# Kernel tuning notes

Measured on AMD Instinct MI355X. Metric: run time of the kernel, lower is better.

Reference implementation:

```python
import jax, jax.numpy as jnp
import numpy as np

NUM_SCALES = 4
ENC = 64
KMAX = 16
DT = 0.005  # base_time_constant; original code's (undefined) self.dt interpreted as this


def setup_inputs() -> dict:
    key = jax.random.key(0)
    ks = jax.random.split(key, 5)
    events = jax.random.normal(ks[0], (2, 2, 32, 32, 64), dtype=jnp.float32)
    # matches torch.logspace(-3, -1, num_scales)
    time_constants = jnp.logspace(-3.0, -1.0, NUM_SCALES).astype(jnp.float32)
    temporal_kernels = jax.random.normal(ks[1], (NUM_SCALES, ENC, KMAX), dtype=jnp.float32)
    w1 = jax.random.normal(ks[2], (2 * NUM_SCALES, NUM_SCALES), dtype=jnp.float32) * 0.1
    b1 = jnp.zeros((2 * NUM_SCALES,), dtype=jnp.float32)
    w2 = jax.random.normal(ks[3], (NUM_SCALES, 2 * NUM_SCALES), dtype=jnp.float32) * 0.1
    b2 = jnp.zeros((NUM_SCALES,), dtype=jnp.float32)
    return {"events": events, "time_constants": time_constants,
            "temporal_kernels": temporal_kernels, "w1": w1, "b1": b1, "w2": w2, "b2": b2}


def reference(events, time_constants, temporal_kernels, w1, b1, w2, b2):
    B, C, H, W, T = events.shape
    k = min(KMAX, T)
    # decay kernels per scale: [S, k], normalized to sum 1
    t_idx = jnp.arange(k, dtype=jnp.float32)
    decay = jnp.exp(-t_idx[None, :] * DT / time_constants[:, None])
    decay = decay / decay.sum(axis=-1, keepdims=True)
    # combined learnable kernels: [S, E, k]
    combined = decay[:, None, :] * temporal_kernels[:, :, :k]

    Cf = C * H * W
    # one batched cross-correlation (torch F.conv1d semantics == lax conv, no flip)
    x = events.reshape(B * Cf, 1, T)                       # [B*Cf, 1, T]
    kern = combined.reshape(NUM_SCALES * ENC, 1, k)        # [S*E, 1, k]
    out = jax.lax.conv_general_dilated(
        x, kern, window_strides=(1,), padding=[(k // 2, k // 2)],
        dimension_numbers=("NCH", "OIH", "NCH"))           # [B*Cf, S*E, T+1]
    Tp = out.shape[-1]
    # [B, E, S, Cf, Tp] matching torch stack order (enc at dim1, scale at dim2)
    feats = out.reshape(B, Cf, NUM_SCALES, ENC, Tp).transpose(0, 3, 2, 1, 4)

    # torch .var() is unbiased -> ddof=1
    feature_variance = feats.var(axis=-1, ddof=1).mean(axis=(1, 3))  # [B, S]
    h = jax.nn.relu(feature_variance @ w1.T + b1)
    attn = jax.nn.softmax(h @ w2.T + b2, axis=-1)                    # [B, S]

    encoded = (feats * attn[:, None, :, None, None]).sum(axis=2)     # [B, E, Cf, Tp]
    return encoded
```

## Files before the change

### kernel.cpp

```cpp
#include <hip/hip_runtime.h>

#define KK 16
#define SS 4
#define EE 64
#define BB 2
#define DT_CONST 0.005f

typedef float f32x4 __attribute__((ext_vector_type(4)));
typedef short bf16x8 __attribute__((ext_vector_type(8)));

#define WS_WK_F 34816

__global__ void __launch_bounds__(512, 1) kA_gram(const float* __restrict__ events,
                                                  float* __restrict__ ws) {
    __shared__ float xs[16][97];
    __shared__ float S1L[16][16];
    __shared__ float part[16][136];
    const int tid = threadIdx.x;

    if (tid < 256) {
        const float4* src = reinterpret_cast<const float4*>(
            events + (size_t)blockIdx.x * 1024);
        float4 v = src[tid];
        int r = tid >> 4, c0 = ((tid & 15) << 2) + 8;
        xs[r][c0] = v.x; xs[r][c0+1] = v.y; xs[r][c0+2] = v.z; xs[r][c0+3] = v.w;
    }
    for (int idx = tid; idx < 16 * 33; idx += 512) {
        int rr = idx / 33, k = idx % 33;
        xs[rr][(k < 8) ? k : (k + 64)] = 0.f;
    }
    __syncthreads();

    const int r   = tid >> 5;
    const int c   = tid & 31;
    const int lag = c >> 1;
    const int h   = c & 1;
    const int off = h * 33;
    const float inv65 = 1.f / 65.f;

    {
        float s = 0.f;
#pragma unroll
        for (int j = 0; j < 32; ++j) s += xs[r][lag + off + j];
        if (!h) s += xs[r][lag + 32];
        s += __shfl_xor(s, 1, 64);
        if (!h) S1L[r][lag] = s;
    }
    __syncthreads();

    {
        float C = 0.f;
#pragma unroll
        for (int j = 0; j < 32; ++j) C += xs[r][off + j] * xs[r][off + j + lag];
        if (!h) C += xs[r][32] * xs[r][32 + lag];
        {
            float Ct = C + __shfl_xor(C, 1, 64);
            if (!h) part[r][lag] = Ct - S1L[r][0] * S1L[r][lag] * inv65;
        }
#pragma unroll
        for (int d1 = 1; d1 <= 15; ++d1) {
            const int add = d1 + off + 32 - h;
            const int rem = d1 - 1 + off;
            C += xs[r][add] * xs[r][add + lag] - xs[r][rem] * xs[r][rem + lag];
            if (lag + d1 <= 15) {
                float Ct = C + __shfl_xor(C, 1, 64);
                if (!h) {
                    int p = 16 * d1 - ((d1 * (d1 - 1)) >> 1) + lag;
                    part[r][p] = Ct - S1L[r][d1] * S1L[r][d1 + lag] * inv65;
                }
            } else {
            }
        }
    }
    __syncthreads();

    if (tid < 136) {
        float g = 0.f;
#pragma unroll
        for (int rr = 0; rr < 16; ++rr) g += part[rr][tid];
        ws[((size_t)((blockIdx.x >> 7) * 136 + tid)) * 128 + (blockIdx.x & 127)] = g;
    }
}

__global__ void __launch_bounds__(256, 1) kM_mlp(const float* __restrict__ tc,
        const float* __restrict__ tk, const float* __restrict__ w1,
        const float* __restrict__ b1, const float* __restrict__ w2,
        const float* __restrict__ b2, float* __restrict__ ws) {
    __shared__ float Gf[2 * 256];
    __shared__ float combL[SS * EE * KK];
    __shared__ float fvL[BB * SS];
    __shared__ float attnL[BB][SS];
    const int tid = threadIdx.x;

    for (int v = tid; v < 272; v += 256) {
        int b = (v >= 136) ? 1 : 0;
        int p = v - b * 136;
        int pp = p, d1 = 0;
        while (pp >= KK - d1) { pp -= KK - d1; ++d1; }
        int d2 = d1 + pp;
        const float4* rp = reinterpret_cast<const float4*>(ws + (size_t)v * 128);
        float acc = 0.f;
#pragma unroll
        for (int i = 0; i < 32; ++i) { float4 q = rp[i]; acc += (q.x + q.y) + (q.z + q.w); }
        Gf[b * 256 + d1 * KK + d2] = acc;
        Gf[b * 256 + d2 * KK + d1] = acc;
    }
    {
        int s = tid >> 6;
        float inv = DT_CONST / tc[s];
        float dk[KK]; float dsum = 0.f;
#pragma unroll
        for (int j = 0; j < KK; ++j) { dk[j] = expf(-(float)j * inv); dsum += dk[j]; }
        float rn = 1.f / dsum;
#pragma unroll
        for (int i = 0; i < 4; ++i) {
            float4 v = reinterpret_cast<const float4*>(tk + tid * KK)[i];
            combL[tid * KK + 4*i + 0] = dk[4*i + 0] * rn * v.x;
            combL[tid * KK + 4*i + 1] = dk[4*i + 1] * rn * v.y;
            combL[tid * KK + 4*i + 2] = dk[4*i + 2] * rn * v.z;
            combL[tid * KK + 4*i + 3] = dk[4*i + 3] * rn * v.w;
        }
    }
    __syncthreads();
    {
        float cvec[KK];
#pragma unroll
        for (int i = 0; i < 4; ++i) {
            float4 v = reinterpret_cast<const float4*>(combL + tid * KK)[i];
            cvec[4*i] = v.x; cvec[4*i+1] = v.y; cvec[4*i+2] = v.z; cvec[4*i+3] = v.w;
        }
        float acc0 = 0.f, acc1 = 0.f;
#pragma unroll
        for (int d1 = 0; d1 < KK; ++d1) {
            float cd1 = cvec[d1];
            float t0 = 0.5f * Gf[d1 * KK + d1] * cd1;
            float t1 = 0.5f * Gf[256 + d1 * KK + d1] * cd1;
#pragma unroll
            for (int d2 = d1 + 1; d2 < KK; ++d2) {
                t0 += Gf[d1 * KK + d2] * cvec[d2];
                t1 += Gf[256 + d1 * KK + d2] * cvec[d2];
            }
            acc0 += 2.f * cd1 * t0;
            acc1 += 2.f * cd1 * t1;
        }
#pragma unroll
        for (int sft = 1; sft < 64; sft <<= 1) {
            acc0 += __shfl_xor(acc0, sft, 64);
            acc1 += __shfl_xor(acc1, sft, 64);
        }
        if ((tid & 63) == 0) {
            const float scale = 1.f / 8388608.f;
            fvL[(tid >> 6)]     = acc0 * scale;
            fvL[4 + (tid >> 6)] = acc1 * scale;
        }
    }
    __syncthreads();
    if (tid < 2) {
        int b = tid;
        float h[8];
#pragma unroll
        for (int i = 0; i < 8; ++i) {
            float a = b1[i];
#pragma unroll
            for (int s = 0; s < SS; ++s) a += fvL[b * SS + s] * w1[i * SS + s];
            h[i] = a > 0.f ? a : 0.f;
        }
        float lg[SS]; float mx = -1e30f;
#pragma unroll
        for (int s = 0; s < SS; ++s) {
            float a = b2[s];
#pragma unroll
            for (int i = 0; i < 8; ++i) a += h[i] * w2[s * 8 + i];
            lg[s] = a; mx = fmaxf(mx, a);
        }
        float se = 0.f;
#pragma unroll
        for (int s = 0; s < SS; ++s) { lg[s] = expf(lg[s] - mx); se += lg[s]; }
#pragma unroll
        for (int s = 0; s < SS; ++s) attnL[b][s] = lg[s] / se;
    }
    __syncthreads();
    {
        unsigned short* wkp = reinterpret_cast<unsigned short*>(ws + WS_WK_F);
#pragma unroll
        for (int j = 0; j < 8; ++j) {
            int o = tid * 8 + j;
            int b = o >> 10, e = (o >> 4) & 63, k = o & 15;
            float a = 0.f;
#pragma unroll
            for (int s = 0; s < SS; ++s)
                a += attnL[b][s] * combL[(s * EE + e) * KK + k];
            unsigned int bits = __float_as_uint(a);
            unsigned short hh = (unsigned short)(bits >> 16);
            float hf = __uint_as_float(((unsigned int)hh) << 16);
            unsigned short ll = (unsigned short)(__float_as_uint(a - hf) >> 16);
            int base = b * 2048 + e * 32 + k;
            wkp[base]          = hh;   wkp[base + 16]        = 0;
            wkp[4096 + base]   = ll;   wkp[4096 + base + 16] = 0;
        }
    }
}

__global__ void __launch_bounds__(256, 8) kC_conv(const float* __restrict__ events,
                                                  const float* __restrict__ ws,
                                                  float* __restrict__ out) {
    __shared__ float xs[2][97];
    __shared__ __align__(16) unsigned short Bh[80 * 24 + 16];
    __shared__ __align__(16) unsigned short Bl[80 * 24 + 16];
    const int tid = threadIdx.x;
    const int bid = blockIdx.x;
    const int b   = bid >> 10;
    const int cf0 = (bid & 1023) << 1;
    const int w   = tid >> 6, l = tid & 63, llo = l & 15, lhi = l >> 4;

    for (int idx = tid; idx < 80 * 24 + 16; idx += 256) { Bh[idx] = 0; Bl[idx] = 0; }

    const unsigned short* wkp = reinterpret_cast<const unsigned short*>(ws + WS_WK_F);
    bf16x8 Ah = *reinterpret_cast<const bf16x8*>(wkp + b * 2048 + (w * 16 + llo) * 32 + 8 * lhi);
    bf16x8 Al = *reinterpret_cast<const bf16x8*>(wkp + 4096 + b * 2048 + (w * 16 + llo) * 32 + 8 * lhi);

    if (tid < 32) {
        float4 v = reinterpret_cast<const float4*>(
            events + ((size_t)b * 2048 + cf0) * 64)[tid];
        int rr = tid >> 4, c0 = ((tid & 15) << 2) + 8;
        xs[rr][c0] = v.x; xs[rr][c0+1] = v.y; xs[rr][c0+2] = v.z; xs[rr][c0+3] = v.w;
    }
    for (int idx = tid; idx < 66; idx += 256) {
        int rr = idx / 33, k = idx % 33;
        xs[rr][(k < 8) ? k : (k + 64)] = 0.f;
    }
    __syncthreads();

#pragma unroll 1
    for (int rr = 0; rr < 2; ++rr) {
#pragma unroll
        for (int q = 0; q < 5; ++q) {
            int idx = tid + q * 256;
            int t = idx >> 4, k = idx & 15;
            float x = xs[rr][t + k];
            unsigned int bits = __float_as_uint(x);
            unsigned short hh = (unsigned short)(bits >> 16);
            float hf = __uint_as_float(((unsigned int)hh) << 16);
            unsigned short ll = (unsigned short)(__float_as_uint(x - hf) >> 16);
            Bh[t * 24 + k] = hh;
            Bl[t * 24 + k] = ll;
        }
        __syncthreads();

        const size_t obase = ((size_t)(b * 64 + w * 16 + lhi * 4) * 2048 + (cf0 + rr)) * 65;
#pragma unroll
        for (int nt = 0; nt < 5; ++nt) {
            bf16x8 Xh = *reinterpret_cast<const bf16x8*>(Bh + (nt * 16 + llo) * 24 + 8 * lhi);
            bf16x8 Xl = *reinterpret_cast<const bf16x8*>(Bl + (nt * 16 + llo) * 24 + 8 * lhi);
            f32x4 acc = {0.f, 0.f, 0.f, 0.f};
            acc = __builtin_amdgcn_mfma_f32_16x16x32_bf16(Al, Xh, acc, 0, 0, 0);
            acc = __builtin_amdgcn_mfma_f32_16x16x32_bf16(Ah, Xl, acc, 0, 0, 0);
            acc = __builtin_amdgcn_mfma_f32_16x16x32_bf16(Ah, Xh, acc, 0, 0, 0);
            const int t0 = nt * 16 + llo;
            if (t0 < 65) {
#pragma unroll
                for (int i = 0; i < 4; ++i)
                    out[obase + (size_t)i * (2048 * 65) + t0] = acc[i];
            }
        }
        __syncthreads();
    }
}

extern "C" void kernel_launch(void* const* d_in, const int* in_sizes, int n_in,
                              void* d_out, int out_size, void* d_ws, size_t ws_size,
                              hipStream_t stream) {
    const float* events = (const float*)d_in[0];
    const float* tc     = (const float*)d_in[1];
    const float* tk     = (const float*)d_in[2];
    const float* w1     = (const float*)d_in[3];
    const float* b1     = (const float*)d_in[4];
    const float* w2     = (const float*)d_in[5];
    const float* b2     = (const float*)d_in[6];
    float* out = (float*)d_out;
    float* ws  = (float*)d_ws;

    hipLaunchKernelGGL(kA_gram, dim3(256),  dim3(512), 0, stream, events, ws);
    hipLaunchKernelGGL(kM_mlp,  dim3(1),    dim3(256), 0, stream, tc, tk, w1, b1, w2, b2, ws);
    hipLaunchKernelGGL(kC_conv, dim3(2048), dim3(256), 0, stream, events, ws, out);
}
```

Measured before the change: 37.95 us.

## Replace MFMA split-bf16 conv with fp32 register sliding-window conv and coalesced stores

The final convolution kernel drops the bf16 hi/lo split MFMA path and computes each output row in fp32 with a 16-tap sliding window held in registers. Each thread covers 16 time steps of one row. Results are staged in shared memory, then written to the output as contiguous float4 stores across a whole 64-row block, instead of scattered scalar stores. The mixing kernel now stores fp32 attention-weighted kernels instead of bf16 pairs. The change trades tensor-core math for plain FMA work, in exchange for fully coalesced writes to the large output.

Measured after the change: 41.47 us. 1.09x slower.

```diff
diff --git a/kernel.cpp b/kernel.cpp
--- a/kernel.cpp
+++ b/kernel.cpp
@@ -1,13 +1,13 @@
 #include <hip/hip_runtime.h>
 
+#define CF 2048
+#define TT 64
+#define TP 65
 #define KK 16
 #define SS 4
 #define EE 64
 #define BB 2
 #define DT_CONST 0.005f
-
-typedef float f32x4 __attribute__((ext_vector_type(4)));
-typedef short bf16x8 __attribute__((ext_vector_type(8)));
 
 #define WS_WK_F 34816
 
@@ -68,7 +68,6 @@
                     int p = 16 * d1 - ((d1 * (d1 - 1)) >> 1) + lag;
                     part[r][p] = Ct - S1L[r][d1] * S1L[r][d1 + lag] * inv65;
                 }
-            } else {
             }
         }
     }
@@ -181,7 +180,6 @@
     }
     __syncthreads();
     {
-        unsigned short* wkp = reinterpret_cast<unsigned short*>(ws + WS_WK_F);
 #pragma unroll
         for (int j = 0; j < 8; ++j) {
             int o = tid * 8 + j;
@@ -190,81 +188,82 @@
 #pragma unroll
             for (int s = 0; s < SS; ++s)
                 a += attnL[b][s] * combL[(s * EE + e) * KK + k];
-            unsigned int bits = __float_as_uint(a);
-            unsigned short hh = (unsigned short)(bits >> 16);
-            float hf = __uint_as_float(((unsigned int)hh) << 16);
-            unsigned short ll = (unsigned short)(__float_as_uint(a - hf) >> 16);
-            int base = b * 2048 + e * 32 + k;
-            wkp[base]          = hh;   wkp[base + 16]        = 0;
-            wkp[4096 + base]   = ll;   wkp[4096 + base + 16] = 0;
-        }
-    }
-}
-
-__global__ void __launch_bounds__(256, 8) kC_conv(const float* __restrict__ events,
+            ws[WS_WK_F + o] = a;
+        }
+    }
+}
+
+__global__ void __launch_bounds__(256, 4) kC_conv(const float* __restrict__ events,
                                                   const float* __restrict__ ws,
                                                   float* __restrict__ out) {
-    __shared__ float xs[2][97];
-    __shared__ __align__(16) unsigned short Bh[80 * 24 + 16];
-    __shared__ __align__(16) unsigned short Bl[80 * 24 + 16];
+    __shared__ float buf[64 * TP];
     const int tid = threadIdx.x;
-    const int bid = blockIdx.x;
-    const int b   = bid >> 10;
-    const int cf0 = (bid & 1023) << 1;
-    const int w   = tid >> 6, l = tid & 63, llo = l & 15, lhi = l >> 4;
-
-    for (int idx = tid; idx < 80 * 24 + 16; idx += 256) { Bh[idx] = 0; Bl[idx] = 0; }
-
-    const unsigned short* wkp = reinterpret_cast<const unsigned short*>(ws + WS_WK_F);
-    bf16x8 Ah = *reinterpret_cast<const bf16x8*>(wkp + b * 2048 + (w * 16 + llo) * 32 + 8 * lhi);
-    bf16x8 Al = *reinterpret_cast<const bf16x8*>(wkp + 4096 + b * 2048 + (w * 16 + llo) * 32 + 8 * lhi);
-
-    if (tid < 32) {
-        float4 v = reinterpret_cast<const float4*>(
-            events + ((size_t)b * 2048 + cf0) * 64)[tid];
-        int rr = tid >> 4, c0 = ((tid & 15) << 2) + 8;
-        xs[rr][c0] = v.x; xs[rr][c0+1] = v.y; xs[rr][c0+2] = v.z; xs[rr][c0+3] = v.w;
-    }
-    for (int idx = tid; idx < 66; idx += 256) {
-        int rr = idx / 33, k = idx % 33;
-        xs[rr][(k < 8) ? k : (k + 64)] = 0.f;
-    }
-    __syncthreads();
-
-#pragma unroll 1
-    for (int rr = 0; rr < 2; ++rr) {
-#pragma unroll
-        for (int q = 0; q < 5; ++q) {
-            int idx = tid + q * 256;
-            int t = idx >> 4, k = idx & 15;
-            float x = xs[rr][t + k];
-            unsigned int bits = __float_as_uint(x);
-            unsigned short hh = (unsigned short)(bits >> 16);
-            float hf = __uint_as_float(((unsigned int)hh) << 16);
-            unsigned short ll = (unsigned short)(__float_as_uint(x - hf) >> 16);
-            Bh[t * 24 + k] = hh;
-            Bl[t * 24 + k] = ll;
-        }
-        __syncthreads();
-
-        const size_t obase = ((size_t)(b * 64 + w * 16 + lhi * 4) * 2048 + (cf0 + rr)) * 65;
-#pragma unroll
-        for (int nt = 0; nt < 5; ++nt) {
-            bf16x8 Xh = *reinterpret_cast<const bf16x8*>(Bh + (nt * 16 + llo) * 24 + 8 * lhi);
-            bf16x8 Xl = *reinterpret_cast<const bf16x8*>(Bl + (nt * 16 + llo) * 24 + 8 * lhi);
-            f32x4 acc = {0.f, 0.f, 0.f, 0.f};
-            acc = __builtin_amdgcn_mfma_f32_16x16x32_bf16(Al, Xh, acc, 0, 0, 0);
-            acc = __builtin_amdgcn_mfma_f32_16x16x32_bf16(Ah, Xl, acc, 0, 0, 0);
-            acc = __builtin_amdgcn_mfma_f32_16x16x32_bf16(Ah, Xh, acc, 0, 0, 0);
-            const int t0 = nt * 16 + llo;
-            if (t0 < 65) {
-#pragma unroll
-                for (int i = 0; i < 4; ++i)
-                    out[obase + (size_t)i * (2048 * 65) + t0] = acc[i];
-            }
-        }
-        __syncthreads();
-    }
+    const int seg = tid >> 6;
+    const int r   = tid & 63;
+    const int c   = blockIdx.x;
+    const int be  = c >> 5;
+    const int rowg = (c << 6) + r;
+    const int b   = be >> 6;
+    const float* xr = events + (((size_t)b << 11) + (rowg & (CF - 1))) * TT;
+
+    float wk[KK];
+#pragma unroll
+    for (int i = 0; i < 4; ++i) {
+        float4 v = reinterpret_cast<const float4*>(ws + WS_WK_F + be * KK)[i];
+        wk[4*i] = v.x; wk[4*i+1] = v.y; wk[4*i+2] = v.z; wk[4*i+3] = v.w;
+    }
+
+    float win[32];
+    if (seg == 0) {
+#pragma unroll
+        for (int k = 0; k < 8; ++k) win[k] = 0.f;
+#pragma unroll
+        for (int k = 0; k < 6; ++k) {
+            float4 v = reinterpret_cast<const float4*>(xr)[k];
+            win[8+4*k] = v.x; win[9+4*k] = v.y; win[10+4*k] = v.z; win[11+4*k] = v.w;
+        }
+    } else if (seg == 3) {
+#pragma unroll
+        for (int k = 0; k < 6; ++k) {
+            float4 v = reinterpret_cast<const float4*>(xr + 40)[k];
+            win[4*k] = v.x; win[4*k+1] = v.y; win[4*k+2] = v.z; win[4*k+3] = v.w;
+        }
+#pragma unroll
+        for (int k = 24; k < 32; ++k) win[k] = 0.f;
+    } else {
+        const float* bp2 = xr + (seg == 1 ? 8 : 24);
+#pragma unroll
+        for (int k = 0; k < 8; ++k) {
+            float4 v = reinterpret_cast<const float4*>(bp2)[k];
+            win[4*k] = v.x; win[4*k+1] = v.y; win[4*k+2] = v.z; win[4*k+3] = v.w;
+        }
+    }
+
+    float acc[16];
+#pragma unroll
+    for (int i = 0; i < 16; ++i) acc[i] = 0.f;
+#pragma unroll
+    for (int dt = 0; dt < 16; ++dt) {
+        float w = wk[dt];
+#pragma unroll
+        for (int i = 0; i < 16; ++i) acc[i] += w * win[i + dt];
+    }
+    float acc16 = 0.f;
+    if (seg == 3) {
+#pragma unroll
+        for (int dt = 0; dt < 8; ++dt) acc16 += wk[dt] * win[16 + dt];
+    }
+
+    float* bp = buf + r * TP + seg * 16;
+#pragma unroll
+    for (int i = 0; i < 16; ++i) bp[i] = acc[i];
+    if (seg == 3) bp[16] = acc16;
+    __syncthreads();
+
+    const float4* bs = reinterpret_cast<const float4*>(buf);
+    float4* od = reinterpret_cast<float4*>(out + (size_t)c * (64 * TP));
+    for (int j = tid; j < 64 * TP / 4; j += 256)
+        od[j] = bs[j];
 }
 
 extern "C" void kernel_launch(void* const* d_in, const int* in_sizes, int n_in,
@@ -282,5 +281,5 @@
 
     hipLaunchKernelGGL(kA_gram, dim3(256),  dim3(512), 0, stream, events, ws);
     hipLaunchKernelGGL(kM_mlp,  dim3(1),    dim3(256), 0, stream, tc, tk, w1, b1, w2, b2, ws);
-    hipLaunchKernelGGL(kC_conv, dim3(2048), dim3(256), 0, stream, events, ws, out);
-}
+    hipLaunchKernelGGL(kC_conv, dim3(4096), dim3(256), 0, stream, events, ws, out);
+}
```

## Split gram kernel into more smaller blocks with four-way lag-sum lanes

Applied to the files above, without the earlier changes.

The gram/variance kernel now runs 1024 blocks of 256 threads, each handling 4 rows instead of 16. Each lag is summed by four lanes over 16-element segments with a two-step shuffle reduction, where before two lanes covered 32-element segments. The aim is better occupancy and shorter serial loops on the many-CU GPU. In exchange, the partial-sum buffer grows fourfold, so the single-block MLP kernel must read and reduce 512 partials per entry instead of 128.

After: 54.06 us. 1.42x slower.

```diff
diff --git a/kernel.cpp b/kernel.cpp
--- a/kernel.cpp
+++ b/kernel.cpp
@@ -9,76 +9,77 @@
 typedef float f32x4 __attribute__((ext_vector_type(4)));
 typedef short bf16x8 __attribute__((ext_vector_type(8)));
 
-#define WS_WK_F 34816
-
-__global__ void __launch_bounds__(512, 1) kA_gram(const float* __restrict__ events,
+#define WS_WK_F 139264
+
+__global__ void __launch_bounds__(256, 4) kA_gram(const float* __restrict__ events,
                                                   float* __restrict__ ws) {
-    __shared__ float xs[16][97];
-    __shared__ float S1L[16][16];
-    __shared__ float part[16][136];
+    __shared__ float xs[4][97];
+    __shared__ float S1L[4][16];
+    __shared__ float part[4][136];
     const int tid = threadIdx.x;
 
-    if (tid < 256) {
+    if (tid < 64) {
         const float4* src = reinterpret_cast<const float4*>(
-            events + (size_t)blockIdx.x * 1024);
+            events + (size_t)blockIdx.x * 256);
         float4 v = src[tid];
         int r = tid >> 4, c0 = ((tid & 15) << 2) + 8;
         xs[r][c0] = v.x; xs[r][c0+1] = v.y; xs[r][c0+2] = v.z; xs[r][c0+3] = v.w;
     }
-    for (int idx = tid; idx < 16 * 33; idx += 512) {
-        int rr = idx / 33, k = idx % 33;
+    if (tid < 132) {
+        int rr = tid / 33, k = tid % 33;
         xs[rr][(k < 8) ? k : (k + 64)] = 0.f;
     }
     __syncthreads();
 
-    const int r   = tid >> 5;
-    const int c   = tid & 31;
-    const int lag = c >> 1;
-    const int h   = c & 1;
-    const int off = h * 33;
+    const int r   = tid >> 6;
+    const int l   = tid & 63;
+    const int lag = l >> 2;
+    const int q   = l & 3;
+    const int off = q << 4;
     const float inv65 = 1.f / 65.f;
 
     {
         float s = 0.f;
 #pragma unroll
-        for (int j = 0; j < 32; ++j) s += xs[r][lag + off + j];
-        if (!h) s += xs[r][lag + 32];
+        for (int j = 0; j < 16; ++j) s += xs[r][lag + off + j];
+        if (q == 3) s += xs[r][lag + 64];
         s += __shfl_xor(s, 1, 64);
-        if (!h) S1L[r][lag] = s;
+        s += __shfl_xor(s, 2, 64);
+        if (q == 0) S1L[r][lag] = s;
     }
     __syncthreads();
 
     {
         float C = 0.f;
 #pragma unroll
-        for (int j = 0; j < 32; ++j) C += xs[r][off + j] * xs[r][off + j + lag];
-        if (!h) C += xs[r][32] * xs[r][32 + lag];
+        for (int j = 0; j < 16; ++j) C += xs[r][off + j] * xs[r][off + j + lag];
+        if (q == 3) C += xs[r][64] * xs[r][64 + lag];
         {
             float Ct = C + __shfl_xor(C, 1, 64);
-            if (!h) part[r][lag] = Ct - S1L[r][0] * S1L[r][lag] * inv65;
-        }
+            Ct += __shfl_xor(Ct, 2, 64);
+            if (q == 0) part[r][lag] = Ct - S1L[r][0] * S1L[r][lag] * inv65;
+        }
+        const int len = 16 + (q == 3 ? 1 : 0);
 #pragma unroll
         for (int d1 = 1; d1 <= 15; ++d1) {
-            const int add = d1 + off + 32 - h;
+            const int add = d1 - 1 + off + len;
             const int rem = d1 - 1 + off;
             C += xs[r][add] * xs[r][add + lag] - xs[r][rem] * xs[r][rem + lag];
             if (lag + d1 <= 15) {
                 float Ct = C + __shfl_xor(C, 1, 64);
-                if (!h) {
+                Ct += __shfl_xor(Ct, 2, 64);
+                if (q == 0) {
                     int p = 16 * d1 - ((d1 * (d1 - 1)) >> 1) + lag;
                     part[r][p] = Ct - S1L[r][d1] * S1L[r][d1 + lag] * inv65;
                 }
-            } else {
             }
         }
     }
     __syncthreads();
 
     if (tid < 136) {
-        float g = 0.f;
-#pragma unroll
-        for (int rr = 0; rr < 16; ++rr) g += part[rr][tid];
-        ws[((size_t)((blockIdx.x >> 7) * 136 + tid)) * 128 + (blockIdx.x & 127)] = g;
+        float g = part[0][tid] + part[1][tid] + part[2][tid] + part[3][tid];
+        ws[((size_t)((blockIdx.x >> 9) * 136 + tid)) * 512 + (blockIdx.x & 511)] = g;
     }
 }
 
@@ -98,10 +99,10 @@
         int pp = p, d1 = 0;
         while (pp >= KK - d1) { pp -= KK - d1; ++d1; }
         int d2 = d1 + pp;
-        const float4* rp = reinterpret_cast<const float4*>(ws + (size_t)v * 128);
+        const float4* rp = reinterpret_cast<const float4*>(ws + (size_t)v * 512);
         float acc = 0.f;
-#pragma unroll
-        for (int i = 0; i < 32; ++i) { float4 q = rp[i]; acc += (q.x + q.y) + (q.z + q.w); }
+#pragma unroll 16
+        for (int i = 0; i < 128; ++i) { float4 qv = rp[i]; acc += (qv.x + qv.y) + (qv.z + qv.w); }
         Gf[b * 256 + d1 * KK + d2] = acc;
         Gf[b * 256 + d2 * KK + d1] = acc;
     }
@@ -280,7 +281,7 @@
     float* out = (float*)d_out;
     float* ws  = (float*)d_ws;
 
-    hipLaunchKernelGGL(kA_gram, dim3(256),  dim3(512), 0, stream, events, ws);
+    hipLaunchKernelGGL(kA_gram, dim3(1024), dim3(256), 0, stream, events, ws);
     hipLaunchKernelGGL(kM_mlp,  dim3(1),    dim3(256), 0, stream, tc, tk, w1, b1, w2, b2, ws);
     hipLaunchKernelGGL(kC_conv, dim3(2048), dim3(256), 0, stream, events, ws, out);
 }
```

## Fuse MLP attention into conv kernel with LDS-staged coalesced output stores

Applied to the files above, without the earlier changes.

Merges the single-block MLP/attention kernel into the convolution kernel, so each of 512 blocks recomputes the Gram-based variance, softmax attention and the bf16 hi/lo weights in LDS instead of reading them from workspace, which removes one kernel launch and its serialization. Each block now handles 8 rows instead of 2. Conv results are staged in LDS and written out row-wise along time for coalescing, with the next row's bf16 split double-buffered. In exchange every block repeats the small MLP work and uses more LDS, which lowers occupancy.

Measured after the change: 37.25 us. Within noise of the previous version (-1.8%).

```diff
diff --git a/kernel.cpp b/kernel.cpp
--- a/kernel.cpp
+++ b/kernel.cpp
@@ -9,7 +9,6 @@
 typedef float f32x4 __attribute__((ext_vector_type(4)));
 typedef short bf16x8 __attribute__((ext_vector_type(8)));
 
-#define WS_WK_F 34816
 
 __global__ void __launch_bounds__(512, 1) kA_gram(const float* __restrict__ events,
                                                   float* __restrict__ ws) {
@@ -68,7 +67,6 @@
                     int p = 16 * d1 - ((d1 * (d1 - 1)) >> 1) + lag;
                     part[r][p] = Ct - S1L[r][d1] * S1L[r][d1 + lag] * inv65;
                 }
-            } else {
             }
         }
     }
@@ -82,19 +80,40 @@
     }
 }
 
-__global__ void __launch_bounds__(256, 1) kM_mlp(const float* __restrict__ tc,
+__global__ void __launch_bounds__(256, 2) kB5_main(
+        const float* __restrict__ events, const float* __restrict__ tc,
         const float* __restrict__ tk, const float* __restrict__ w1,
         const float* __restrict__ b1, const float* __restrict__ w2,
-        const float* __restrict__ b2, float* __restrict__ ws) {
-    __shared__ float Gf[2 * 256];
-    __shared__ float combL[SS * EE * KK];
-    __shared__ float fvL[BB * SS];
-    __shared__ float attnL[BB][SS];
+        const float* __restrict__ b2, const float* __restrict__ ws,
+        float* __restrict__ out) {
+    __shared__ float stage[2][4352];
+    __shared__ float xs[8 * 97];
+    __shared__ __align__(16) unsigned short wkh[64 * 32];
+    __shared__ __align__(16) unsigned short wkl[64 * 32];
+    __shared__ __align__(16) unsigned short Bh[2][1936];
+    __shared__ __align__(16) unsigned short Bl[2][1936];
+    float* Gf    = stage[0];
+    float* fvL   = stage[0] + 512;
+    float* combL = stage[1];
     const int tid = threadIdx.x;
-
+    const int bid = blockIdx.x;
+    const int b   = bid >> 8;
+    const int w   = tid >> 6, l = tid & 63, llo = l & 15, lhi = l >> 4;
+
+    for (int idx = tid; idx < 2 * 1936; idx += 256) { Bh[0][idx] = 0; Bl[0][idx] = 0; }
+    for (int idx = tid; idx < 8 * 33; idx += 256) {
+        int rr = idx / 33, k = idx % 33;
+        xs[rr * 97 + ((k < 8) ? k : (k + 64))] = 0.f;
+    }
+    if (tid < 128) {
+        float4 v = reinterpret_cast<const float4*>(events + (size_t)bid * 512)[tid];
+        int rr = tid >> 4, c0 = ((tid & 15) << 2) + 8;
+        xs[rr * 97 + c0] = v.x; xs[rr * 97 + c0 + 1] = v.y;
+        xs[rr * 97 + c0 + 2] = v.z; xs[rr * 97 + c0 + 3] = v.w;
+    }
     for (int v = tid; v < 272; v += 256) {
-        int b = (v >= 136) ? 1 : 0;
-        int p = v - b * 136;
+        int b2i = (v >= 136) ? 1 : 0;
+        int p  = v - b2i * 136;
         int pp = p, d1 = 0;
         while (pp >= KK - d1) { pp -= KK - d1; ++d1; }
         int d2 = d1 + pp;
@@ -102,8 +121,8 @@
         float acc = 0.f;
 #pragma unroll
         for (int i = 0; i < 32; ++i) { float4 q = rp[i]; acc += (q.x + q.y) + (q.z + q.w); }
-        Gf[b * 256 + d1 * KK + d2] = acc;
-        Gf[b * 256 + d2 * KK + d1] = acc;
+        Gf[(b2i * KK + d1) * KK + d2] = acc;
+        Gf[(b2i * KK + d2) * KK + d1] = acc;
     }
     {
         int s = tid >> 6;
@@ -122,6 +141,7 @@
         }
     }
     __syncthreads();
+
     {
         float cvec[KK];
 #pragma unroll
@@ -155,14 +175,17 @@
         }
     }
     __syncthreads();
-    if (tid < 2) {
-        int b = tid;
+
+    {
+        float fv[SS];
+#pragma unroll
+        for (int s = 0; s < SS; ++s) fv[s] = fvL[b * SS + s];
         float h[8];
 #pragma unroll
         for (int i = 0; i < 8; ++i) {
             float a = b1[i];
 #pragma unroll
-            for (int s = 0; s < SS; ++s) a += fvL[b * SS + s] * w1[i * SS + s];
+            for (int s = 0; s < SS; ++s) a += fv[s] * w1[i * SS + s];
             h[i] = a > 0.f ? a : 0.f;
         }
         float lg[SS]; float mx = -1e30f;
@@ -176,94 +199,98 @@
         float se = 0.f;
 #pragma unroll
         for (int s = 0; s < SS; ++s) { lg[s] = expf(lg[s] - mx); se += lg[s]; }
-#pragma unroll
-        for (int s = 0; s < SS; ++s) attnL[b][s] = lg[s] / se;
-    }
-    __syncthreads();
-    {
-        unsigned short* wkp = reinterpret_cast<unsigned short*>(ws + WS_WK_F);
-#pragma unroll
-        for (int j = 0; j < 8; ++j) {
-            int o = tid * 8 + j;
-            int b = o >> 10, e = (o >> 4) & 63, k = o & 15;
+        float attn[SS];
+#pragma unroll
+        for (int s = 0; s < SS; ++s) attn[s] = lg[s] / se;
+#pragma unroll
+        for (int j = 0; j < 4; ++j) {
+            int idx = tid * 4 + j;
+            int e = idx >> 4, k2 = idx & 15;
             float a = 0.f;
 #pragma unroll
             for (int s = 0; s < SS; ++s)
-                a += attnL[b][s] * combL[(s * EE + e) * KK + k];
+                a += attn[s] * combL[(s * EE + e) * KK + k2];
             unsigned int bits = __float_as_uint(a);
             unsigned short hh = (unsigned short)(bits >> 16);
             float hf = __uint_as_float(((unsigned int)hh) << 16);
             unsigned short ll = (unsigned short)(__float_as_uint(a - hf) >> 16);
-            int base = b * 2048 + e * 32 + k;
-            wkp[base]          = hh;   wkp[base + 16]        = 0;
-            wkp[4096 + base]   = ll;   wkp[4096 + base + 16] = 0;
-        }
-    }
-}
-
-__global__ void __launch_bounds__(256, 8) kC_conv(const float* __restrict__ events,
-                                                  const float* __restrict__ ws,
-                                                  float* __restrict__ out) {
-    __shared__ float xs[2][97];
-    __shared__ __align__(16) unsigned short Bh[80 * 24 + 16];
-    __shared__ __align__(16) unsigned short Bl[80 * 24 + 16];
-    const int tid = threadIdx.x;
-    const int bid = blockIdx.x;
-    const int b   = bid >> 10;
-    const int cf0 = (bid & 1023) << 1;
-    const int w   = tid >> 6, l = tid & 63, llo = l & 15, lhi = l >> 4;
-
-    for (int idx = tid; idx < 80 * 24 + 16; idx += 256) { Bh[idx] = 0; Bl[idx] = 0; }
-
-    const unsigned short* wkp = reinterpret_cast<const unsigned short*>(ws + WS_WK_F);
-    bf16x8 Ah = *reinterpret_cast<const bf16x8*>(wkp + b * 2048 + (w * 16 + llo) * 32 + 8 * lhi);
-    bf16x8 Al = *reinterpret_cast<const bf16x8*>(wkp + 4096 + b * 2048 + (w * 16 + llo) * 32 + 8 * lhi);
-
-    if (tid < 32) {
-        float4 v = reinterpret_cast<const float4*>(
-            events + ((size_t)b * 2048 + cf0) * 64)[tid];
-        int rr = tid >> 4, c0 = ((tid & 15) << 2) + 8;
-        xs[rr][c0] = v.x; xs[rr][c0+1] = v.y; xs[rr][c0+2] = v.z; xs[rr][c0+3] = v.w;
-    }
-    for (int idx = tid; idx < 66; idx += 256) {
-        int rr = idx / 33, k = idx % 33;
-        xs[rr][(k < 8) ? k : (k + 64)] = 0.f;
-    }
-    __syncthreads();
+            wkh[e * 32 + k2] = hh;      wkl[e * 32 + k2] = ll;
+            wkh[e * 32 + 16 + k2] = 0;  wkl[e * 32 + 16 + k2] = 0;
+        }
+    }
+#pragma unroll
+    for (int q = 0; q < 5; ++q) {
+        int idx = tid + q * 256;
+        int t = idx >> 4, k = idx & 15;
+        float x = xs[t + k];
+        unsigned int bits = __float_as_uint(x);
+        unsigned short hh = (unsigned short)(bits >> 16);
+        float hf = __uint_as_float(((unsigned int)hh) << 16);
+        unsigned short ll = (unsigned short)(__float_as_uint(x - hf) >> 16);
+        Bh[0][t * 24 + k] = hh;
+        Bl[0][t * 24 + k] = ll;
+    }
+    __syncthreads();
+
+    bf16x8 Ah = *reinterpret_cast<const bf16x8*>(&wkh[(w * 16 + llo) * 32 + 8 * lhi]);
+    bf16x8 Al = *reinterpret_cast<const bf16x8*>(&wkl[(w * 16 + llo) * 32 + 8 * lhi]);
+    const size_t obase0 = ((size_t)b * 64 * 2048 + (size_t)(bid & 255) * 8) * 65;
 
 #pragma unroll 1
-    for (int rr = 0; rr < 2; ++rr) {
-#pragma unroll
-        for (int q = 0; q < 5; ++q) {
-            int idx = tid + q * 256;
-            int t = idx >> 4, k = idx & 15;
-            float x = xs[rr][t + k];
-            unsigned int bits = __float_as_uint(x);
-            unsigned short hh = (unsigned short)(bits >> 16);
-            float hf = __uint_as_float(((unsigned int)hh) << 16);
-            unsigned short ll = (unsigned short)(__float_as_uint(x - hf) >> 16);
-            Bh[t * 24 + k] = hh;
-            Bl[t * 24 + k] = ll;
-        }
-        __syncthreads();
-
-        const size_t obase = ((size_t)(b * 64 + w * 16 + lhi * 4) * 2048 + (cf0 + rr)) * 65;
+    for (int cf = 0; cf < 8; ++cf) {
+        const int cur = cf & 1;
 #pragma unroll
         for (int nt = 0; nt < 5; ++nt) {
-            bf16x8 Xh = *reinterpret_cast<const bf16x8*>(Bh + (nt * 16 + llo) * 24 + 8 * lhi);
-            bf16x8 Xl = *reinterpret_cast<const bf16x8*>(Bl + (nt * 16 + llo) * 24 + 8 * lhi);
+            bf16x8 Xh = *reinterpret_cast<const bf16x8*>(&Bh[cur][(nt * 16 + llo) * 24 + 8 * lhi]);
+            bf16x8 Xl = *reinterpret_cast<const bf16x8*>(&Bl[cur][(nt * 16 + llo) * 24 + 8 * lhi]);
             f32x4 acc = {0.f, 0.f, 0.f, 0.f};
             acc = __builtin_amdgcn_mfma_f32_16x16x32_bf16(Al, Xh, acc, 0, 0, 0);
             acc = __builtin_amdgcn_mfma_f32_16x16x32_bf16(Ah, Xl, acc, 0, 0, 0);
             acc = __builtin_amdgcn_mfma_f32_16x16x32_bf16(Ah, Xh, acc, 0, 0, 0);
-            const int t0 = nt * 16 + llo;
-            if (t0 < 65) {
+            if (nt < 4 || llo < 4) {
 #pragma unroll
                 for (int i = 0; i < 4; ++i)
-                    out[obase + (size_t)i * (2048 * 65) + t0] = acc[i];
-            }
+                    stage[cur][(w * 16 + lhi * 4 + i) * 68 + nt * 16 + llo] = acc[i];
+            }
+        }
+        if (cf < 7) {
+            const float* xrow = xs + (cf + 1) * 97;
+#pragma unroll
+            for (int q = 0; q < 5; ++q) {
+                int idx = tid + q * 256;
+                int t = idx >> 4, k = idx & 15;
+                float x = xrow[t + k];
+                unsigned int bits = __float_as_uint(x);
+                unsigned short hh = (unsigned short)(bits >> 16);
+                float hf = __uint_as_float(((unsigned int)hh) << 16);
+                unsigned short ll = (unsigned short)(__float_as_uint(x - hf) >> 16);
+                Bh[cur ^ 1][t * 24 + k] = hh;
+                Bl[cur ^ 1][t * 24 + k] = ll;
+            }
+        }
+        if (cf > 0) {
+            const float* sg = stage[cur ^ 1];
+            const size_t ob = obase0 + (size_t)(cf - 1) * 65;
+            int q = tid >> 6, tloc = tid & 63;
+#pragma unroll
+            for (int kk = 0; kk < 16; ++kk) {
+                int e = q * 16 + kk;
+                out[ob + (size_t)e * 133120 + tloc] = sg[e * 68 + tloc];
+            }
+            if (tid < 64) out[ob + (size_t)tid * 133120 + 64] = sg[tid * 68 + 64];
         }
         __syncthreads();
+    }
+    {
+        const float* sg = stage[1];
+        const size_t ob = obase0 + (size_t)7 * 65;
+        int q = tid >> 6, tloc = tid & 63;
+#pragma unroll
+        for (int kk = 0; kk < 16; ++kk) {
+            int e = q * 16 + kk;
+            out[ob + (size_t)e * 133120 + tloc] = sg[e * 68 + tloc];
+        }
+        if (tid < 64) out[ob + (size_t)tid * 133120 + 64] = sg[tid * 68 + 64];
     }
 }
 
@@ -280,7 +307,7 @@
     float* out = (float*)d_out;
     float* ws  = (float*)d_ws;
 
-    hipLaunchKernelGGL(kA_gram, dim3(256),  dim3(512), 0, stream, events, ws);
-    hipLaunchKernelGGL(kM_mlp,  dim3(1),    dim3(256), 0, stream, tc, tk, w1, b1, w2, b2, ws);
-    hipLaunchKernelGGL(kC_conv, dim3(2048), dim3(256), 0, stream, events, ws, out);
+    hipLaunchKernelGGL(kA_gram,  dim3(256), dim3(512), 0, stream, events, ws);
+    hipLaunchKernelGGL(kB5_main, dim3(512), dim3(256), 0, stream,
+                       events, tc, tk, w1, b1, w2, b2, ws, out);
 }
```
